# Kernel tuning notes

Hardware: AMD Instinct MI355X
Metric: run time of the kernel (lower is better)

Reference implementation:

```python
import jax, jax.numpy as jnp
import numpy as np

B, S, D, H, DK = 2, 2048, 256, 8, 32


def setup_inputs() -> dict:
    key = jax.random.key(0)
    ks = jax.random.split(key, 12)
    inp = {
        "query": jax.random.normal(ks[0], (B, S, D), jnp.float32),
        "key_": jax.random.normal(ks[1], (B, S, D), jnp.float32),
        "value": jax.random.normal(ks[2], (B, S, D), jnp.float32),
        "mask": jax.random.randint(ks[3], (B, S, S), 0, 2).astype(bool),
        "relation": jax.random.normal(ks[4], (B, S, S), jnp.float32) * 0.05,
        # learned params (Linear stores y = x @ W^T; we store W already transposed)
        "Wq": jax.random.normal(ks[5], (D, H * DK), jnp.float32) * 0.02,
        "Wk": jax.random.normal(ks[6], (D, H * DK), jnp.float32) * 0.02,
        "Wv": jax.random.normal(ks[7], (D, H * DK), jnp.float32) * 0.02,
        "Wfc": jax.random.normal(ks[8], (H * DK, D), jnp.float32) * 0.02,
        "bfc": jax.random.normal(ks[9], (D,), jnp.float32) * 0.02,
        "gamma": jnp.ones((D,), jnp.float32),
        "beta": jnp.zeros((D,), jnp.float32),
    }
    return inp


def _layernorm(x, gamma, beta, eps=1e-5):
    mu = jnp.mean(x, axis=-1, keepdims=True)
    var = jnp.var(x, axis=-1, keepdims=True)
    return (x - mu) * jax.lax.rsqrt(var + eps) * gamma + beta


def reference(query, key_, value, mask, relation, Wq, Wk, Wv, Wfc, bfc, gamma, beta):
    b, s, _ = query.shape
    def split_heads(x, W):
        return (x @ W).reshape(b, s, H, DK).transpose(0, 2, 1, 3)  # [B,H,S,DK]
    Q = split_heads(query, Wq)
    K = split_heads(key_, Wk)
    V = split_heads(value, Wv)
    # (Q K^T) @ relation / sqrt(dk)   -- relation broadcast over heads
    qk = jnp.einsum('bhqd,bhkd->bhqk', Q, K)          # [B,H,S,S]
    scores = jnp.einsum('bhqk,bkn->bhqn', qk, relation) / jnp.sqrt(jnp.float32(DK))
    scores = jnp.where(mask[:, None, :, :], jnp.float32(-1e9), scores)
    attn = jax.nn.softmax(scores, axis=-1)            # dropout in eval mode = identity
    att = jnp.einsum('bhqn,bhnd->bhqd', attn, V)      # [B,H,S,DK]
    att = att.transpose(0, 2, 1, 3).reshape(b, s, H * DK)
    out = att @ Wfc + bfc
    return _layernorm(out + query, gamma, beta), attn
```

## Files before the change

### kernel.cpp

```cpp
#include <hip/hip_runtime.h>

constexpr int Bc = 2, Sc = 2048, Dc = 256, Hc = 8, DKc = 32;
constexpr int BH = Bc * Hc;

typedef _Float16 f16x8 __attribute__((ext_vector_type(8)));
typedef _Float16 f16x4 __attribute__((ext_vector_type(4)));
typedef float    f32x4 __attribute__((ext_vector_type(4)));

__global__ __launch_bounds__(256) void proj_kernel(
    const float* __restrict__ X, const float* __restrict__ W,
    _Float16* __restrict__ out, int vtrans, float scale)
{
    constexpr int ROWS = 8;
    __shared__ float xs[ROWS][Dc];
    const int r0 = blockIdx.x * ROWS;
    const int t = threadIdx.x;
    #pragma unroll
    for (int i = 0; i < ROWS; ++i)
        xs[i][t] = X[(long)(r0 + i) * Dc + t];
    __syncthreads();
    float acc[ROWS];
    #pragma unroll
    for (int i = 0; i < ROWS; ++i) acc[i] = 0.f;
    for (int d = 0; d < Dc; ++d) {
        float w = W[d * Dc + t];
        #pragma unroll
        for (int i = 0; i < ROWS; ++i) acc[i] = fmaf(xs[i][d], w, acc[i]);
    }
    const int h = t >> 5, dk = t & 31;
    #pragma unroll
    for (int i = 0; i < ROWS; ++i) {
        int row = r0 + i;
        int b = row / Sc, s = row % Sc;
        long idx = vtrans ? (((long)(b * Hc + h) * DKc + dk) * Sc + s)
                          : (((long)(b * Hc + h) * Sc + s) * DKc + dk);
        out[idx] = (_Float16)(acc[i] * scale);
    }
}

__global__ __launch_bounds__(256) void relT_kernel(
    const float* __restrict__ rel, _Float16* __restrict__ relT)
{
    __shared__ float tile[64][65];
    const int b = blockIdx.z;
    const int k0 = blockIdx.y * 64, n0 = blockIdx.x * 64;
    const int tx = threadIdx.x & 63, ty = threadIdx.x >> 6;
    const float* src = rel + (long)b * Sc * Sc;
    #pragma unroll
    for (int i = 0; i < 16; ++i) {
        int k = i * 4 + ty;
        tile[k][tx] = src[(long)(k0 + k) * Sc + n0 + tx];
    }
    __syncthreads();
    _Float16* dst = relT + (long)b * Sc * Sc;
    #pragma unroll
    for (int i = 0; i < 16; ++i) {
        int n = i * 4 + ty;
        dst[(long)(n0 + n) * Sc + k0 + tx] = (_Float16)tile[tx][n];
    }
}

__global__ __launch_bounds__(256) void maskpack_kernel(
    const unsigned int* __restrict__ m, unsigned int* __restrict__ out)
{
    const int idx = blockIdx.x * 256 + threadIdx.x;
    const uint4 a = ((const uint4*)m)[idx * 2];
    const uint4 b = ((const uint4*)m)[idx * 2 + 1];
    unsigned int ws[8] = {a.x, a.y, a.z, a.w, b.x, b.y, b.z, b.w};
    unsigned int r = 0;
    #pragma unroll
    for (int j = 0; j < 8; ++j) {
        unsigned int nib = (ws[j] | (ws[j] >> 7) | (ws[j] >> 14) | (ws[j] >> 21)) & 0xFu;
        r |= nib << (4 * j);
    }
    out[idx] = r;
}

__global__ __launch_bounds__(256) void kr_kernel(
    const _Float16* __restrict__ relT, const _Float16* __restrict__ Kt,
    _Float16* __restrict__ KRT)
{
    constexpr int LDK = 72;
    __shared__ _Float16 As[64][LDK];
    __shared__ _Float16 Bs[64][LDK];
    const int b = blockIdx.z;
    const int m0 = blockIdx.y * 64;
    const int n0 = blockIdx.x * 64;
    const _Float16* Ap = relT + (long)b * Sc * Sc;
    const _Float16* Bp = Kt + (long)b * Hc * DKc * Sc;
    const int t = threadIdx.x;
    const int lane = t & 63, wave = t >> 6;
    const int wr = wave >> 1, wc = wave & 1;
    const int c = lane & 15, g = lane >> 4;
    const int lrow = t >> 2;
    const int lcol = (t & 3) * 16;
    f32x4 acc[2][2] = {};
    for (int k0 = 0; k0 < Sc; k0 += 64) {
        *(f16x8*)&As[lrow][lcol]     = *(const f16x8*)&Ap[(long)(m0 + lrow) * Sc + k0 + lcol];
        *(f16x8*)&As[lrow][lcol + 8] = *(const f16x8*)&Ap[(long)(m0 + lrow) * Sc + k0 + lcol + 8];
        *(f16x8*)&Bs[lrow][lcol]     = *(const f16x8*)&Bp[(long)(n0 + lrow) * Sc + k0 + lcol];
        *(f16x8*)&Bs[lrow][lcol + 8] = *(const f16x8*)&Bp[(long)(n0 + lrow) * Sc + k0 + lcol + 8];
        __syncthreads();
        #pragma unroll
        for (int kk = 0; kk < 2; ++kk) {
            const int kb = kk * 32 + g * 8;
            f16x8 af[2], bf[2];
            #pragma unroll
            for (int m = 0; m < 2; ++m)
                af[m] = *(const f16x8*)&As[wr * 32 + m * 16 + c][kb];
            #pragma unroll
            for (int n = 0; n < 2; ++n)
                bf[n] = *(const f16x8*)&Bs[wc * 32 + n * 16 + c][kb];
            #pragma unroll
            for (int m = 0; m < 2; ++m)
                #pragma unroll
                for (int n = 0; n < 2; ++n)
                    acc[m][n] = __builtin_amdgcn_mfma_f32_16x16x32_f16(
                        af[m], bf[n], acc[m][n], 0, 0, 0);
        }
        __syncthreads();
    }
    _Float16* outp = KRT + (long)b * Sc * 256;
    #pragma unroll
    for (int m = 0; m < 2; ++m)
        #pragma unroll
        for (int n = 0; n < 2; ++n)
            #pragma unroll
            for (int i = 0; i < 4; ++i) {
                int row = m0 + wr * 32 + m * 16 + g * 4 + i;
                int col = n0 + wc * 32 + n * 16 + c;
                outp[(long)row * 256 + col] = (_Float16)acc[m][n][i];
            }
}

__global__ __launch_bounds__(256) void fused_attn_kernel(
    const _Float16* __restrict__ Qb,
    const _Float16* __restrict__ KRT,
    const _Float16* __restrict__ Vt,
    const unsigned int* __restrict__ mbits,
    float* __restrict__ attn_out,
    float* __restrict__ attw)
{
    constexpr int NT = 128, LDA = 132, LDP = 136;
    __shared__ float    a_lds[64][LDA];
    __shared__ _Float16 p_lds[64][LDP];
    const int bh = blockIdx.y;
    const int b = bh >> 3, h = bh & 7;
    const int q0 = blockIdx.x * 64;
    const int t = threadIdx.x, lane = t & 63, w = t >> 6;
    const int c = lane & 15, g = lane >> 4;
    const int q = q0 + w * 16 + c;
    const f16x8 qf = *(const f16x8*)&Qb[((long)bh * Sc + q) * DKc + g * 8];
    const _Float16* krt = KRT + (long)b * Sc * 256 + h * 32;
    const unsigned int* mbitrow = mbits + ((long)b * Sc + q) * (Sc / 32);
    const f32x4 zero = {};

    float esum = 0.f;
    for (int nt = 0; nt < Sc / NT; ++nt) {
        const int n0 = nt * NT;
        f32x4 s[8];
        #pragma unroll
        for (int nf = 0; nf < 8; ++nf) {
            f16x8 kf = *(const f16x8*)&krt[(long)(n0 + nf * 16 + c) * 256 + g * 8];
            s[nf] = __builtin_amdgcn_mfma_f32_16x16x32_f16(kf, qf, zero, 0, 0, 0);
        }
        const uint4 mq = *(const uint4*)&mbitrow[nt * 4];
        const unsigned int mwv[4] = {mq.x, mq.y, mq.z, mq.w};
        #pragma unroll
        for (int nf = 0; nf < 8; ++nf) {
            const unsigned int bits = mwv[nf >> 1] >> ((nf & 1) * 16 + g * 4);
            #pragma unroll
            for (int i = 0; i < 4; ++i) {
                float sv = ((bits >> i) & 1u) ? -1e9f : s[nf][i];
                esum += __expf(sv);
            }
        }
    }
    esum += __shfl_xor(esum, 16);
    esum += __shfl_xor(esum, 32);
    const float rinv = 1.f / esum;

    f32x4 acc[2] = {};
    float* aoutw = attn_out + (long)bh * Sc * Sc
                 + (long)(q0 + w * 16 + (lane >> 5)) * Sc + (lane & 31) * 4;
    for (int nt = 0; nt < Sc / NT; ++nt) {
        const int n0 = nt * NT;
        f32x4 s[8];
        #pragma unroll
        for (int nf = 0; nf < 8; ++nf) {
            f16x8 kf = *(const f16x8*)&krt[(long)(n0 + nf * 16 + c) * 256 + g * 8];
            s[nf] = __builtin_amdgcn_mfma_f32_16x16x32_f16(kf, qf, zero, 0, 0, 0);
        }
        const uint4 mq = *(const uint4*)&mbitrow[nt * 4];
        const unsigned int mwv[4] = {mq.x, mq.y, mq.z, mq.w};
        #pragma unroll
        for (int nf = 0; nf < 8; ++nf) {
            const unsigned int bits = mwv[nf >> 1] >> ((nf & 1) * 16 + g * 4);
            f32x4 av;
            f16x4 pv;
            #pragma unroll
            for (int i = 0; i < 4; ++i) {
                float sv = ((bits >> i) & 1u) ? -1e9f : s[nf][i];
                float a = __expf(sv) * rinv;
                av[i] = a;
                pv[i] = (_Float16)a;
            }
            *(f32x4*)&a_lds[w * 16 + c][nf * 16 + g * 4] = av;
            *(f16x4*)&p_lds[w * 16 + c][nf * 16 + g * 4] = pv;
        }
        #pragma unroll
        for (int r2 = 0; r2 < 8; ++r2) {
            f32x4 v = *(const f32x4*)&a_lds[w * 16 + r2 * 2 + (lane >> 5)][(lane & 31) * 4];
            __builtin_nontemporal_store(v, (f32x4*)&aoutw[(long)(r2 * 2) * Sc + n0]);
        }
        #pragma unroll
        for (int ks = 0; ks < 4; ++ks) {
            f16x8 af = *(const f16x8*)&p_lds[w * 16 + c][ks * 32 + g * 8];
            #pragma unroll
            for (int nb = 0; nb < 2; ++nb) {
                f16x8 vf = *(const f16x8*)&Vt[((long)bh * DKc + nb * 16 + c) * Sc + n0 + ks * 32 + g * 8];
                acc[nb] = __builtin_amdgcn_mfma_f32_16x16x32_f16(af, vf, acc[nb], 0, 0, 0);
            }
        }
    }
    #pragma unroll
    for (int nb = 0; nb < 2; ++nb)
        #pragma unroll
        for (int i = 0; i < 4; ++i)
            attw[((long)(b * Sc + q0 + w * 16 + g * 4 + i)) * Dc + h * 32 + nb * 16 + c] = acc[nb][i];
}

__global__ __launch_bounds__(256) void out_kernel(
    const float* __restrict__ att, const float* __restrict__ Wfc,
    const float* __restrict__ bfc, const float* __restrict__ query,
    const float* __restrict__ gamma, const float* __restrict__ beta,
    float* __restrict__ out)
{
    __shared__ float xs[4][Dc];
    __shared__ float ys[4][Dc];
    const int r0 = blockIdx.x * 4;
    const int t = threadIdx.x;
    #pragma unroll
    for (int i = 0; i < 4; ++i) xs[i][t] = att[(long)(r0 + i) * Dc + t];
    __syncthreads();
    float acc[4] = {0.f, 0.f, 0.f, 0.f};
    for (int d = 0; d < Dc; ++d) {
        float wv = Wfc[d * Dc + t];
        #pragma unroll
        for (int i = 0; i < 4; ++i) acc[i] = fmaf(xs[i][d], wv, acc[i]);
    }
    const float bias = bfc[t];
    #pragma unroll
    for (int i = 0; i < 4; ++i)
        ys[i][t] = acc[i] + bias + query[(long)(r0 + i) * Dc + t];
    __syncthreads();
    const int w = t >> 6, lane = t & 63;
    float x0 = ys[w][lane], x1 = ys[w][lane + 64];
    float x2 = ys[w][lane + 128], x3 = ys[w][lane + 192];
    float sum = x0 + x1 + x2 + x3;
    float sq = x0 * x0 + x1 * x1 + x2 * x2 + x3 * x3;
    for (int off = 32; off; off >>= 1) {
        sum += __shfl_down(sum, off);
        sq  += __shfl_down(sq, off);
    }
    sum = __shfl(sum, 0);
    sq  = __shfl(sq, 0);
    const float mu = sum * (1.f / 256.f);
    const float var = sq * (1.f / 256.f) - mu * mu;
    const float rstd = rsqrtf(var + 1e-5f);
    float* orow = out + (long)(r0 + w) * Dc;
    orow[lane]       = (x0 - mu) * rstd * gamma[lane]       + beta[lane];
    orow[lane + 64]  = (x1 - mu) * rstd * gamma[lane + 64]  + beta[lane + 64];
    orow[lane + 128] = (x2 - mu) * rstd * gamma[lane + 128] + beta[lane + 128];
    orow[lane + 192] = (x3 - mu) * rstd * gamma[lane + 192] + beta[lane + 192];
}

extern "C" void kernel_launch(void* const* d_in, const int* in_sizes, int n_in,
                              void* d_out, int out_size, void* d_ws, size_t ws_size,
                              hipStream_t stream)
{
    const float* query   = (const float*)d_in[0];
    const float* key_    = (const float*)d_in[1];
    const float* value   = (const float*)d_in[2];
    const unsigned int* mask = (const unsigned int*)d_in[3];
    const float* relation = (const float*)d_in[4];
    const float* Wq  = (const float*)d_in[5];
    const float* Wk  = (const float*)d_in[6];
    const float* Wv  = (const float*)d_in[7];
    const float* Wfc = (const float*)d_in[8];
    const float* bfc = (const float*)d_in[9];
    const float* gamma = (const float*)d_in[10];
    const float* beta  = (const float*)d_in[11];

    float* out_ln   = (float*)d_out;
    float* out_attn = (float*)d_out + (size_t)Bc * Sc * Dc;

    char* ws = (char*)d_ws;
    _Float16* Qb   = (_Float16*)(ws + 0);
    _Float16* Kt   = (_Float16*)(ws + 2097152);
    _Float16* Vt   = (_Float16*)(ws + 4194304);
    _Float16* relT = (_Float16*)(ws + 6291456);
    _Float16* KRT  = (_Float16*)(ws + 23068672);
    float*    attw = (float*)   (ws + 25165824);
    unsigned int* mbits = (unsigned int*)(ws + 29360128);

    const float qscale = 0.17677669529663689f;
    proj_kernel<<<dim3(Bc * Sc / 8), 256, 0, stream>>>(query, Wq, Qb, 0, qscale);
    proj_kernel<<<dim3(Bc * Sc / 8), 256, 0, stream>>>(key_, Wk, Kt, 1, 1.0f);
    proj_kernel<<<dim3(Bc * Sc / 8), 256, 0, stream>>>(value, Wv, Vt, 1, 1.0f);
    relT_kernel<<<dim3(Sc / 64, Sc / 64, Bc), 256, 0, stream>>>(relation, relT);
    maskpack_kernel<<<dim3(Bc * Sc * Sc / 32 / 256), 256, 0, stream>>>(mask, mbits);
    kr_kernel<<<dim3(4, Sc / 64, Bc), 256, 0, stream>>>(relT, Kt, KRT);
    fused_attn_kernel<<<dim3(Sc / 64, BH), 256, 0, stream>>>(
        Qb, KRT, Vt, mbits, out_attn, attw);
    out_kernel<<<dim3(Bc * Sc / 4), 256, 0, stream>>>(attw, Wfc, bfc, query,
                                                      gamma, beta, out_ln);
}
```

Baseline: 234.2 us.

## Single-pass attention caching unnormalized probabilities in registers; merge QKV projections

```diff
diff --git a/kernel.cpp b/kernel.cpp
--- a/kernel.cpp
+++ b/kernel.cpp
@@ -7,12 +7,22 @@
 typedef _Float16 f16x4 __attribute__((ext_vector_type(4)));
 typedef float    f32x4 __attribute__((ext_vector_type(4)));
 
-__global__ __launch_bounds__(256) void proj_kernel(
-    const float* __restrict__ X, const float* __restrict__ W,
-    _Float16* __restrict__ out, int vtrans, float scale)
+__global__ __launch_bounds__(256) void proj3_kernel(
+    const float* __restrict__ query, const float* __restrict__ key_,
+    const float* __restrict__ value, const float* __restrict__ Wq,
+    const float* __restrict__ Wk, const float* __restrict__ Wv,
+    _Float16* __restrict__ Qb, _Float16* __restrict__ Kt,
+    _Float16* __restrict__ Vt)
 {
     constexpr int ROWS = 8;
     __shared__ float xs[ROWS][Dc];
+    const int z = blockIdx.y;
+    const float* X = (z == 0) ? query : (z == 1) ? key_ : value;
+    const float* W = (z == 0) ? Wq : (z == 1) ? Wk : Wv;
+    _Float16* out = (z == 0) ? Qb : (z == 1) ? Kt : Vt;
+    const int vtrans = (z != 0);
+    const float scale = (z == 0) ? 0.17677669529663689f : 1.0f;
+
     const int r0 = blockIdx.x * ROWS;
     const int t = threadIdx.x;
     #pragma unroll
@@ -141,8 +151,7 @@
     float* __restrict__ attn_out,
     float* __restrict__ attw)
 {
-    constexpr int NT = 128, LDA = 132, LDP = 136;
-    __shared__ float    a_lds[64][LDA];
+    constexpr int NT = 128, NTILES = Sc / NT, LDP = 136;
     __shared__ _Float16 p_lds[64][LDP];
     const int bh = blockIdx.y;
     const int b = bh >> 3, h = bh & 7;
@@ -155,8 +164,12 @@
     const unsigned int* mbitrow = mbits + ((long)b * Sc + q) * (Sc / 32);
     const f32x4 zero = {};
 
+    f16x4 p_regs[NTILES][8];
+    f32x4 acc[2] = {};
     float esum = 0.f;
-    for (int nt = 0; nt < Sc / NT; ++nt) {
+
+    #pragma unroll
+    for (int nt = 0; nt < NTILES; ++nt) {
         const int n0 = nt * NT;
         f32x4 s[8];
         #pragma unroll
@@ -169,49 +182,16 @@
         #pragma unroll
         for (int nf = 0; nf < 8; ++nf) {
             const unsigned int bits = mwv[nf >> 1] >> ((nf & 1) * 16 + g * 4);
+            f16x4 pv;
             #pragma unroll
             for (int i = 0; i < 4; ++i) {
                 float sv = ((bits >> i) & 1u) ? -1e9f : s[nf][i];
-                esum += __expf(sv);
+                float p = __expf(sv);
+                esum += p;
+                pv[i] = (_Float16)p;
             }
-        }
-    }
-    esum += __shfl_xor(esum, 16);
-    esum += __shfl_xor(esum, 32);
-    const float rinv = 1.f / esum;
-
-    f32x4 acc[2] = {};
-    float* aoutw = attn_out + (long)bh * Sc * Sc
-                 + (long)(q0 + w * 16 + (lane >> 5)) * Sc + (lane & 31) * 4;
-    for (int nt = 0; nt < Sc / NT; ++nt) {
-        const int n0 = nt * NT;
-        f32x4 s[8];
-        #pragma unroll
-        for (int nf = 0; nf < 8; ++nf) {
-            f16x8 kf = *(const f16x8*)&krt[(long)(n0 + nf * 16 + c) * 256 + g * 8];
-            s[nf] = __builtin_amdgcn_mfma_f32_16x16x32_f16(kf, qf, zero, 0, 0, 0);
-        }
-        const uint4 mq = *(const uint4*)&mbitrow[nt * 4];
-        const unsigned int mwv[4] = {mq.x, mq.y, mq.z, mq.w};
-        #pragma unroll
-        for (int nf = 0; nf < 8; ++nf) {
-            const unsigned int bits = mwv[nf >> 1] >> ((nf & 1) * 16 + g * 4);
-            f32x4 av;
-            f16x4 pv;
-            #pragma unroll
-            for (int i = 0; i < 4; ++i) {
-                float sv = ((bits >> i) & 1u) ? -1e9f : s[nf][i];
-                float a = __expf(sv) * rinv;
-                av[i] = a;
-                pv[i] = (_Float16)a;
-            }
-            *(f32x4*)&a_lds[w * 16 + c][nf * 16 + g * 4] = av;
+            p_regs[nt][nf] = pv;
             *(f16x4*)&p_lds[w * 16 + c][nf * 16 + g * 4] = pv;
-        }
-        #pragma unroll
-        for (int r2 = 0; r2 < 8; ++r2) {
-            f32x4 v = *(const f32x4*)&a_lds[w * 16 + r2 * 2 + (lane >> 5)][(lane & 31) * 4];
-            __builtin_nontemporal_store(v, (f32x4*)&aoutw[(long)(r2 * 2) * Sc + n0]);
         }
         #pragma unroll
         for (int ks = 0; ks < 4; ++ks) {
@@ -223,11 +203,36 @@
             }
         }
     }
+    esum += __shfl_xor(esum, 16);
+    esum += __shfl_xor(esum, 32);
+    const float rinv = 1.f / esum;
+
+    float* aoutw = attn_out + (long)bh * Sc * Sc
+                 + (long)(q0 + w * 16 + (lane >> 5)) * Sc + (lane & 31) * 4;
+    #pragma unroll
+    for (int nt = 0; nt < NTILES; ++nt) {
+        #pragma unroll
+        for (int nf = 0; nf < 8; ++nf)
+            *(f16x4*)&p_lds[w * 16 + c][nf * 16 + g * 4] = p_regs[nt][nf];
+        #pragma unroll
+        for (int r2 = 0; r2 < 8; ++r2) {
+            const int lrow = r2 * 2 + (lane >> 5);
+            f16x4 pv = *(const f16x4*)&p_lds[w * 16 + lrow][(lane & 31) * 4];
+            const float rs = __shfl(rinv, lrow);
+            f32x4 av;
+            #pragma unroll
+            for (int i = 0; i < 4; ++i) av[i] = (float)pv[i] * rs;
+            __builtin_nontemporal_store(av, (f32x4*)&aoutw[(long)(r2 * 2) * Sc + nt * NT]);
+        }
+    }
     #pragma unroll
     for (int nb = 0; nb < 2; ++nb)
         #pragma unroll
-        for (int i = 0; i < 4; ++i)
-            attw[((long)(b * Sc + q0 + w * 16 + g * 4 + i)) * Dc + h * 32 + nb * 16 + c] = acc[nb][i];
+        for (int i = 0; i < 4; ++i) {
+            const float rs = __shfl(rinv, g * 4 + i);
+            attw[((long)(b * Sc + q0 + w * 16 + g * 4 + i)) * Dc + h * 32 + nb * 16 + c]
+                = acc[nb][i] * rs;
+        }
 }
 
 __global__ __launch_bounds__(256) void out_kernel(
@@ -304,10 +309,8 @@
     float*    attw = (float*)   (ws + 25165824);
     unsigned int* mbits = (unsigned int*)(ws + 29360128);
 
-    const float qscale = 0.17677669529663689f;
-    proj_kernel<<<dim3(Bc * Sc / 8), 256, 0, stream>>>(query, Wq, Qb, 0, qscale);
-    proj_kernel<<<dim3(Bc * Sc / 8), 256, 0, stream>>>(key_, Wk, Kt, 1, 1.0f);
-    proj_kernel<<<dim3(Bc * Sc / 8), 256, 0, stream>>>(value, Wv, Vt, 1, 1.0f);
+    proj3_kernel<<<dim3(Bc * Sc / 8, 3), 256, 0, stream>>>(
+        query, key_, value, Wq, Wk, Wv, Qb, Kt, Vt);
     relT_kernel<<<dim3(Sc / 64, Sc / 64, Bc), 256, 0, stream>>>(relation, relT);
     maskpack_kernel<<<dim3(Bc * Sc * Sc / 32 / 256), 256, 0, stream>>>(mask, mbits);
     kr_kernel<<<dim3(4, Sc / 64, Bc), 256, 0, stream>>>(relT, Kt, KRT);
```

Result: slower. 276.5 us (+18.0%).
